# Kernel tuning notes

Hardware: AMD Instinct MI355X
Metric: run time of the kernel (lower is better)

## Reference

```python
import jax, jax.numpy as jnp
import numpy as np

B = 16384       # batch of Monte-Carlo paths
NSTEPS = 32     # time discretization N
H = 128         # hidden width of sub-networks
L = 1.0         # sphere radius l
T1 = 1.0
T0 = 0.0
DT = float((T1 - T0) / NSTEPS)


def _mlp(n, x, W1, b1, W2, b2):
    # sub-network on concat([N, X]): (B,1)+(B,3) -> (B,out)
    inp = jnp.concatenate([n, x], axis=-1)
    h = jnp.tanh(inp @ W1.T + b1)
    return h @ W2.T + b2


def _forward(process_N, process_X, discrete_t, delta_B,
             rW1, rb1, rW2, rb2, gW1, gb1, gW2, gb2, jW1, jb1, jW2, jb2):
    eye = jnp.eye(3, dtype=process_X.dtype)
    alpha = 0.3 * jax.nn.sigmoid(0.1 * process_N)    # birth intensity, (N+1,B,1)
    beta = 0.2 * jax.nn.sigmoid(-0.1 * process_N)    # death intensity, (N+1,B,1)
    u0 = _mlp(process_N[0], process_X[0], rW1, rb1, rW2, rb2)  # result net, (B,1)

    def step(u, xs):
        (Ni, Xi, Np1, ti, dB, ai, bi,
         gW1i, gb1i, gW2i, gb2i, jW1i, jb1i, jW2i, jb2i) = xs
        grad_u = _mlp(Ni, Xi, gW1i, gb1i, gW2i, gb2i)           # (B,3)
        outer = Xi[:, :, None] * Xi[:, None, :] / (L * L)       # (B,3,3)
        sigma = jnp.swapaxes(eye - outer, -2, -1)               # sigma0(X)^T
        T_inv = eye + outer
        k = jnp.sqrt(2.0 / (1.0 + 0.1 * Ni * Ni)) / L           # sqrt(2 D(N))/l, (B,1)
        kg = k * grad_u
        grad_bmm = jnp.einsum('bi,bij,bjk,bk->b', kg, T_inv, sigma, dB)[:, None]
        ui = _mlp(Ni, Xi, jW1i, jb1i, jW2i, jb2i)
        uip = _mlp(Ni + 1.0, Xi, jW1i, jb1i, jW2i, jb2i)
        uim = _mlp(Ni - 1.0, Xi, jW1i, jb1i, jW2i, jb2i)
        dp = uip - ui
        dm = uim - ui
        f = -0.05 * u + 0.05 * jnp.sum(grad_u * Xi, -1, keepdims=True) / L + 0.01 * ti
        u = u + grad_bmm - (ai * dp + bi * dm) * DT - f * DT
        dN = jnp.round(Np1 - Ni)
        u = u + jnp.where(dN > 0, dp, 0.0) + jnp.where(dN < 0, dm, 0.0)
        return u, None

    xs = (process_N[:-1], process_X[:-1], process_N[1:], discrete_t[:-1], delta_B,
          alpha[:-1], beta[:-1], gW1, gb1, gW2, gb2, jW1, jb1, jW2, jb2)
    u, _ = jax.lax.scan(step, u0, xs)
    g = 0.1 * process_N[-1] + jnp.cos(process_X[-1][:, :1])    # terminal condition
    return u, g


def setup_inputs():
    key = jax.random.key(0)
    ks = jax.random.split(key, 16)
    # integer-valued jump process N_t (kept float32), increments in {-1,0,1}
    n0 = jax.random.randint(ks[0], (1, B, 1), 5, 15).astype(jnp.float32)
    jumps = jax.random.randint(ks[1], (NSTEPS, B, 1), -1, 2).astype(jnp.float32)
    process_N = jnp.concatenate([n0, n0 + jnp.cumsum(jumps, axis=0)], axis=0)
    # spatial process on the sphere of radius L
    xr = jax.random.normal(ks[2], (NSTEPS + 1, B, 3), dtype=jnp.float32)
    process_X = L * xr / jnp.linalg.norm(xr, axis=-1, keepdims=True)
    discrete_t = jnp.linspace(T0, T1, NSTEPS + 1, dtype=jnp.float32)
    delta_B = jax.random.normal(ks[3], (NSTEPS, B, 3), dtype=jnp.float32) * float(np.sqrt(DT))

    def lin(k, shape, fan_in):
        return jax.random.normal(k, shape, dtype=jnp.float32) / float(np.sqrt(fan_in))

    rW1 = lin(ks[4], (H, 4), 4);           rb1 = jnp.zeros((H,), jnp.float32)
    rW2 = lin(ks[5], (1, H), H);           rb2 = jnp.zeros((1,), jnp.float32)
    gW1 = lin(ks[6], (NSTEPS, H, 4), 4);   gb1 = jnp.zeros((NSTEPS, H), jnp.float32)
    gW2 = lin(ks[7], (NSTEPS, 3, H), H);   gb2 = jnp.zeros((NSTEPS, 3), jnp.float32)
    jW1 = lin(ks[8], (NSTEPS, H, 4), 4);   jb1 = jnp.zeros((NSTEPS, H), jnp.float32)
    jW2 = lin(ks[9], (NSTEPS, 1, H), H);   jb2 = jnp.zeros((NSTEPS, 1), jnp.float32)
    return dict(process_N=process_N, process_X=process_X, discrete_t=discrete_t,
                delta_B=delta_B, rW1=rW1, rb1=rb1, rW2=rW2, rb2=rb2,
                gW1=gW1, gb1=gb1, gW2=gW2, gb2=gb2,
                jW1=jW1, jb1=jb1, jW2=jW2, jb2=jb2)


def reference(process_N, process_X, discrete_t, delta_B,
              rW1, rb1, rW2, rb2, gW1, gb1, gW2, gb2, jW1, jb1, jW2, jb2):
    return _forward(process_N, process_X, discrete_t, delta_B,
                    rW1, rb1, rW2, rb2, gW1, gb1, gW2, gb2, jW1, jb1, jW2, jb2)
```

## Files before the change

### kernel.cpp

```cpp
#include <hip/hip_runtime.h>
#include <math.h>

#define BB 16384
#define NSTEPS 32
#define HH 128
#define DTF (1.0f/32.0f)
#define SCALE 2.88539008177792681f
#define LOG2E 1.44269504088896340f

typedef float v2f __attribute__((ext_vector_type(2)));
typedef float v16f __attribute__((ext_vector_type(16)));
typedef unsigned int v2u __attribute__((ext_vector_type(2)));

#define SL(v,k) (__builtin_shufflevector((v),(v),2*(k),2*(k)+1))

__device__ __forceinline__ v2f pk_fma(v2f a, v2f b, v2f c) {
    return __builtin_elementwise_fma(a, b, c);
}

__device__ __forceinline__ v2f pk_rcp1(v2f x) {
    v2u xb; __builtin_memcpy(&xb, &x, 8);
    v2u yb = (v2u){0x7EF311C3u, 0x7EF311C3u} - xb;
    v2f y;  __builtin_memcpy(&y, &yb, 8);
    v2f u = pk_fma(-x, y, (v2f){2.0f, 2.0f});
    return y * u;
}

__device__ __forceinline__ float fexp2(float x) {
#if __has_builtin(__builtin_amdgcn_exp2f)
    return __builtin_amdgcn_exp2f(x);
#else
    float r; asm("v_exp_f32 %0, %1" : "=v"(r) : "v"(x)); return r;
#endif
}
__device__ __forceinline__ float frcp(float x) {
#if __has_builtin(__builtin_amdgcn_rcpf)
    return __builtin_amdgcn_rcpf(x);
#else
    float r; asm("v_rcp_f32 %0, %1" : "=v"(r) : "v"(x)); return r;
#endif
}
__device__ __forceinline__ float frsq(float x) {
#if __has_builtin(__builtin_amdgcn_rsqf)
    return __builtin_amdgcn_rsqf(x);
#else
    float r; asm("v_rsq_f32 %0, %1" : "=v"(r) : "v"(x)); return r;
#endif
}

__global__ __launch_bounds__(HH) void xform_kernel(
    const float* __restrict__ gW1, const float* __restrict__ gb1,
    const float* __restrict__ gW2, const float* __restrict__ gb2,
    const float* __restrict__ jW1, const float* __restrict__ jb1,
    const float* __restrict__ jW2,
    float* __restrict__ recA, float* __restrict__ G)
{
    const int i = blockIdx.x;
    const int j = threadIdx.x;
    const int pair = j >> 1;
    const int ln   = j & 1;
    float* r = recA + ((size_t)i*64 + pair)*32;

    const float* gw = gW1 + (size_t)(i*HH + j)*4;
    const float* jw = jW1 + (size_t)(i*HH + j)*4;
    float jw0 = jw[0];
    float g20 = gW2[i*3*HH + 0*HH + j];
    float g21 = gW2[i*3*HH + 1*HH + j];
    float g22 = gW2[i*3*HH + 2*HH + j];

    r[ 0+ln] = SCALE*gw[0];
    r[ 2+ln] = SCALE*gw[1];
    r[ 4+ln] = SCALE*gw[2];
    r[ 6+ln] = SCALE*gw[3];
    r[ 8+ln] = SCALE*gb1[i*HH + j];
    r[10+ln] = -2.0f*g20;
    r[12+ln] = -2.0f*g21;
    r[14+ln] = -2.0f*g22;

    r[16+ln] = SCALE*jw0;
    r[18+ln] = SCALE*jw[1];
    r[20+ln] = SCALE*jw[2];
    r[22+ln] = SCALE*jw[3];
    r[24+ln] = SCALE*jb1[i*HH + j];
    r[26+ln] = -2.0f*jW2[i*HH + j];
    r[28+ln] = exp2f( SCALE*jw0);
    r[30+ln] = exp2f(-SCALE*jw0);

    __shared__ float sh[3*HH];
    sh[0*HH + j] = g20; sh[1*HH + j] = g21; sh[2*HH + j] = g22;
    __syncthreads();
    if (j < 3) {
        float s = gb2[i*3 + j];
        for (int t = 0; t < HH; ++t) s += sh[j*HH + t];
        G[i*4 + j] = s;
    }
}

__global__ __launch_bounds__(256) void step_kernel(
    const float* __restrict__ N, const float* __restrict__ X,
    const float* __restrict__ T, const float* __restrict__ dB,
    const float* __restrict__ recA, const float* __restrict__ G,
    float* __restrict__ C)
{
    const int tid  = threadIdx.x;
    const int i    = blockIdx.x >> 8;
    const int bblk = blockIdx.x & 255;
    const int bl   = tid & 63;
    const int jq   = __builtin_amdgcn_readfirstlane(tid >> 6);
    const int b    = bblk*64 + bl;
    const int ib   = i*BB + b;

    const float Ni = N[ib];
    const float x0 = X[(size_t)ib*3 + 0], x1 = X[(size_t)ib*3 + 1], x2 = X[(size_t)ib*3 + 2];

    const v16f* rec16 = (const v16f*)(recA + (size_t)i*HH*16 + (size_t)jq*512);

    const v2f Niv  = {Ni, Ni};
    const v2f x0v  = {x0, x0};
    const v2f x1v  = {x1, x1};
    const v2f x2v  = {x2, x2};
    const v2f onev = {1.0f, 1.0f};
    const v2f c25v = {25.0f, 25.0f};

    v2f ga0 = {0.f,0.f}, ga1 = {0.f,0.f}, ga2 = {0.f,0.f};
    v2f a0  = {0.f,0.f}, aP  = {0.f,0.f}, aM  = {0.f,0.f};

#pragma unroll 2
    for (int t = 0; t < 16; ++t) {
        const v16f Rg = rec16[2*t + 0];
        const v16f Rj = rec16[2*t + 1];

        v2f ag = SL(Rg,4) * onev;
        ag = pk_fma(SL(Rg,0), Niv, ag);
        ag = pk_fma(SL(Rg,1), x0v, ag);
        ag = pk_fma(SL(Rg,2), x1v, ag);
        ag = pk_fma(SL(Rg,3), x2v, ag);
        ag = __builtin_elementwise_min(ag, c25v);
        v2f eg; eg.x = fexp2(ag.x); eg.y = fexp2(ag.y);
        v2f rg = pk_rcp1(eg + 1.0f);
        ga0 = pk_fma(SL(Rg,5), rg, ga0);
        ga1 = pk_fma(SL(Rg,6), rg, ga1);
        ga2 = pk_fma(SL(Rg,7), rg, ga2);

        v2f aj = SL(Rj,4) * onev;
        aj = pk_fma(SL(Rj,0), Niv, aj);
        aj = pk_fma(SL(Rj,1), x0v, aj);
        aj = pk_fma(SL(Rj,2), x1v, aj);
        aj = pk_fma(SL(Rj,3), x2v, aj);
        aj = __builtin_elementwise_min(aj, c25v);
        v2f ej; ej.x = fexp2(aj.x); ej.y = fexp2(aj.y);
        v2f r0 = pk_rcp1(ej + 1.0f);
        v2f rp = pk_rcp1(pk_fma(SL(Rj,6), ej, onev));
        v2f rm = pk_rcp1(pk_fma(SL(Rj,7), ej, onev));
        const v2f w2p = SL(Rj,5);
        a0 = pk_fma(w2p, r0, a0);
        aP = pk_fma(w2p, rp, aP);
        aM = pk_fma(w2p, rm, aM);
    }

    const float hga0 = ga0.x + ga0.y;
    const float hga1 = ga1.x + ga1.y;
    const float hga2 = ga2.x + ga2.y;
    const float ha0  = a0.x  + a0.y;
    const float haP  = aP.x  + aP.y;
    const float haM  = aM.x  + aM.y;

    __shared__ float sh[3][6][64];
    if (jq) {
        float* s = &sh[jq-1][0][bl];
        s[0*64] = hga0; s[1*64] = hga1; s[2*64] = hga2;
        s[3*64] = ha0;  s[4*64] = haP;  s[5*64] = haM;
    }
    __syncthreads();
    if (!jq) {
        float v0 = hga0, v1 = hga1, v2 = hga2;
        float v3 = ha0,  v4 = haP,  v5 = haM;
#pragma unroll
        for (int q = 0; q < 3; ++q) {
            v0 += sh[q][0][bl]; v1 += sh[q][1][bl]; v2 += sh[q][2][bl];
            v3 += sh[q][3][bl]; v4 += sh[q][4][bl]; v5 += sh[q][5][bl];
        }
        const float g0 = G[i*4 + 0] + v0;
        const float g1 = G[i*4 + 1] + v1;
        const float g2 = G[i*4 + 2] + v2;
        const float A0 = v3;
        const float AP = v4;
        const float AM = v5;

        const float Np1 = N[ib + BB];
        const float d0 = dB[(size_t)ib*3 + 0], d1 = dB[(size_t)ib*3 + 1], d2 = dB[(size_t)ib*3 + 2];
        const float ti = T[i];

        const float gdx = g0*x0 + g1*x1 + g2*x2;
        const float ss  = x0*x0 + x1*x1 + x2*x2;
        const float gdB = g0*d0 + g1*d1 + g2*d2;
        const float xdB = x0*d0 + x1*d1 + x2*d2;

        const float k = 1.41421356237309505f * frsq(fmaf(0.1f*Ni, Ni, 1.0f));
        const float grad_bmm = k * (gdB - ss*gdx*xdB);

        const float dp = AP - A0;
        const float dm = AM - A0;

        const float sig = frcp(1.0f + fexp2(-0.1f*LOG2E*Ni));
        const float alpha = 0.3f*sig;
        const float beta  = 0.2f - 0.2f*sig;

        const float dd = Np1 - Ni;
        const float jump = (dd > 0.5f) ? dp : ((dd < -0.5f) ? dm : 0.0f);

        const float c = grad_bmm - (alpha*dp + beta*dm)*DTF
                      - 0.05f*DTF*gdx - 0.01f*DTF*ti + jump;
        C[ib] = c;
    }
}

__global__ __launch_bounds__(256) void final_kernel(
    const float* __restrict__ N, const float* __restrict__ X,
    const float* __restrict__ rW1, const float* __restrict__ rb1,
    const float* __restrict__ rW2, const float* __restrict__ rb2,
    const float* __restrict__ C, float* __restrict__ out)
{
    const int gid = blockIdx.x*256 + threadIdx.x;
    const int b = gid >> 4;
    const int p = gid & 15;

    const float n0 = N[b];
    const float x0 = X[(size_t)b*3 + 0], x1 = X[(size_t)b*3 + 1], x2 = X[(size_t)b*3 + 2];

    float accw = 0.f, accr = 0.f;
#pragma unroll
    for (int t = 0; t < 8; ++t) {
        const int j = p*8 + t;
        float pre = fmaf(rW1[j*4+0], n0, fmaf(rW1[j*4+1], x0,
                    fmaf(rW1[j*4+2], x1, fmaf(rW1[j*4+3], x2, rb1[j]))));
        float r  = frcp(1.0f + fexp2(SCALE*pre));
        float w2 = rW2[j];
        accw += w2;
        accr = fmaf(w2, r, accr);
    }
    accw += __shfl_down(accw, 8, 16);  accr += __shfl_down(accr, 8, 16);
    accw += __shfl_down(accw, 4, 16);  accr += __shfl_down(accr, 4, 16);
    accw += __shfl_down(accw, 2, 16);  accr += __shfl_down(accr, 2, 16);
    accw += __shfl_down(accw, 1, 16);  accr += __shfl_down(accr, 1, 16);

    if (p == 0) {
        float u = rb2[0] + accw - 2.0f*accr;

        const float sfac = 1.0f + 0.05f*DTF;
#pragma unroll
        for (int i = 0; i < NSTEPS; ++i)
            u = fmaf(u, sfac, C[(size_t)i*BB + b]);
        out[b] = u;

        const int ib = NSTEPS*BB + b;
        out[BB + b] = fmaf(0.1f, N[ib], __cosf(X[(size_t)ib*3]));
    }
}

extern "C" void kernel_launch(void* const* d_in, const int* in_sizes, int n_in,
                              void* d_out, int out_size, void* d_ws, size_t ws_size,
                              hipStream_t stream)
{
    const float* N   = (const float*)d_in[0];
    const float* X   = (const float*)d_in[1];
    const float* T   = (const float*)d_in[2];
    const float* dB  = (const float*)d_in[3];
    const float* rW1 = (const float*)d_in[4];
    const float* rb1 = (const float*)d_in[5];
    const float* rW2 = (const float*)d_in[6];
    const float* rb2 = (const float*)d_in[7];
    const float* gW1 = (const float*)d_in[8];
    const float* gb1 = (const float*)d_in[9];
    const float* gW2 = (const float*)d_in[10];
    const float* gb2 = (const float*)d_in[11];
    const float* jW1 = (const float*)d_in[12];
    const float* jb1 = (const float*)d_in[13];
    const float* jW2 = (const float*)d_in[14];

    float* ws   = (float*)d_ws;
    float* C    = ws;
    float* recA = ws + (size_t)NSTEPS*BB;
    float* G    = recA + (size_t)NSTEPS*HH*16;
    float* out  = (float*)d_out;

    xform_kernel<<<NSTEPS, HH, 0, stream>>>(gW1, gb1, gW2, gb2, jW1, jb1, jW2, recA, G);
    step_kernel<<<NSTEPS*(BB/64), 256, 0, stream>>>(N, X, T, dB, recA, G, C);
    final_kernel<<<BB*16/256, 256, 0, stream>>>(N, X, rW1, rb1, rW2, rb2, C, out);
}
```

Baseline: 63.75 us.

## Split hidden units across 8 waves and parallelize final recurrence and bias reductions

The step kernel now uses 512 threads per block, so each of 8 waves handles 16 hidden units (fully unrolled) instead of 4 waves handling 32, and the shared-memory partial reduction grows to 7 slots. The final kernel replaces the serial 32-step linear recurrence with a closed-form weighted sum: each of 16 lanes loads two C values scaled by precomputed powers of (1+0.05*DT), and the results are reduced with shuffles. The xform kernel's serial bias sum becomes a tree reduction. This buys more latency hiding and shorter per-thread chains at the cost of more block-level reduction work and slightly different floating-point summation order.

```diff
diff --git a/kernel.cpp b/kernel.cpp
--- a/kernel.cpp
+++ b/kernel.cpp
@@ -8,7 +8,7 @@
 #define SCALE 2.88539008177792681f
 #define LOG2E 1.44269504088896340f
 
-typedef float v2f __attribute__((ext_vector_type(2)));
+typedef float v2f  __attribute__((ext_vector_type(2)));
 typedef float v16f __attribute__((ext_vector_type(16)));
 typedef unsigned int v2u __attribute__((ext_vector_type(2)));
 
@@ -87,16 +87,20 @@
     r[30+ln] = exp2f(-SCALE*jw0);
 
     __shared__ float sh[3*HH];
-    sh[0*HH + j] = g20; sh[1*HH + j] = g21; sh[2*HH + j] = g22;
+    sh[j] = g20; sh[HH + j] = g21; sh[2*HH + j] = g22;
     __syncthreads();
-    if (j < 3) {
-        float s = gb2[i*3 + j];
-        for (int t = 0; t < HH; ++t) s += sh[j*HH + t];
-        G[i*4 + j] = s;
-    }
-}
-
-__global__ __launch_bounds__(256) void step_kernel(
+    for (int off = 64; off >= 1; off >>= 1) {
+        if (j < off) {
+            sh[j]      += sh[j + off];
+            sh[HH + j] += sh[HH + j + off];
+            sh[2*HH+j] += sh[2*HH + j + off];
+        }
+        __syncthreads();
+    }
+    if (j < 3) G[i*4 + j] = gb2[i*3 + j] + sh[j*HH];
+}
+
+__global__ __launch_bounds__(512) void step_kernel(
     const float* __restrict__ N, const float* __restrict__ X,
     const float* __restrict__ T, const float* __restrict__ dB,
     const float* __restrict__ recA, const float* __restrict__ G,
@@ -106,14 +110,14 @@
     const int i    = blockIdx.x >> 8;
     const int bblk = blockIdx.x & 255;
     const int bl   = tid & 63;
-    const int jq   = __builtin_amdgcn_readfirstlane(tid >> 6);
+    const int je   = __builtin_amdgcn_readfirstlane(tid >> 6);
     const int b    = bblk*64 + bl;
     const int ib   = i*BB + b;
 
     const float Ni = N[ib];
     const float x0 = X[(size_t)ib*3 + 0], x1 = X[(size_t)ib*3 + 1], x2 = X[(size_t)ib*3 + 2];
 
-    const v16f* rec16 = (const v16f*)(recA + (size_t)i*HH*16 + (size_t)jq*512);
+    const v16f* rec16 = (const v16f*)(recA + (size_t)i*HH*16 + (size_t)je*256);
 
     const v2f Niv  = {Ni, Ni};
     const v2f x0v  = {x0, x0};
@@ -125,31 +129,31 @@
     v2f ga0 = {0.f,0.f}, ga1 = {0.f,0.f}, ga2 = {0.f,0.f};
     v2f a0  = {0.f,0.f}, aP  = {0.f,0.f}, aM  = {0.f,0.f};
 
-#pragma unroll 2
-    for (int t = 0; t < 16; ++t) {
+#pragma unroll
+    for (int t = 0; t < 8; ++t) {
         const v16f Rg = rec16[2*t + 0];
         const v16f Rj = rec16[2*t + 1];
 
-        v2f ag = SL(Rg,4) * onev;
+        v2f ag = SL(Rg,4);
         ag = pk_fma(SL(Rg,0), Niv, ag);
         ag = pk_fma(SL(Rg,1), x0v, ag);
         ag = pk_fma(SL(Rg,2), x1v, ag);
         ag = pk_fma(SL(Rg,3), x2v, ag);
         ag = __builtin_elementwise_min(ag, c25v);
         v2f eg; eg.x = fexp2(ag.x); eg.y = fexp2(ag.y);
-        v2f rg = pk_rcp1(eg + 1.0f);
+        v2f rg = pk_rcp1(eg + onev);
         ga0 = pk_fma(SL(Rg,5), rg, ga0);
         ga1 = pk_fma(SL(Rg,6), rg, ga1);
         ga2 = pk_fma(SL(Rg,7), rg, ga2);
 
-        v2f aj = SL(Rj,4) * onev;
+        v2f aj = SL(Rj,4);
         aj = pk_fma(SL(Rj,0), Niv, aj);
         aj = pk_fma(SL(Rj,1), x0v, aj);
         aj = pk_fma(SL(Rj,2), x1v, aj);
         aj = pk_fma(SL(Rj,3), x2v, aj);
         aj = __builtin_elementwise_min(aj, c25v);
         v2f ej; ej.x = fexp2(aj.x); ej.y = fexp2(aj.y);
-        v2f r0 = pk_rcp1(ej + 1.0f);
+        v2f r0 = pk_rcp1(ej + onev);
         v2f rp = pk_rcp1(pk_fma(SL(Rj,6), ej, onev));
         v2f rm = pk_rcp1(pk_fma(SL(Rj,7), ej, onev));
         const v2f w2p = SL(Rj,5);
@@ -165,27 +169,24 @@
     const float haP  = aP.x  + aP.y;
     const float haM  = aM.x  + aM.y;
 
-    __shared__ float sh[3][6][64];
-    if (jq) {
-        float* s = &sh[jq-1][0][bl];
+    __shared__ float sh[7][6][64];
+    if (je) {
+        float* s = &sh[je-1][0][bl];
         s[0*64] = hga0; s[1*64] = hga1; s[2*64] = hga2;
         s[3*64] = ha0;  s[4*64] = haP;  s[5*64] = haM;
     }
     __syncthreads();
-    if (!jq) {
+    if (!je) {
         float v0 = hga0, v1 = hga1, v2 = hga2;
         float v3 = ha0,  v4 = haP,  v5 = haM;
 #pragma unroll
-        for (int q = 0; q < 3; ++q) {
+        for (int q = 0; q < 7; ++q) {
             v0 += sh[q][0][bl]; v1 += sh[q][1][bl]; v2 += sh[q][2][bl];
             v3 += sh[q][3][bl]; v4 += sh[q][4][bl]; v5 += sh[q][5][bl];
         }
         const float g0 = G[i*4 + 0] + v0;
         const float g1 = G[i*4 + 1] + v1;
         const float g2 = G[i*4 + 2] + v2;
-        const float A0 = v3;
-        const float AP = v4;
-        const float AM = v5;
 
         const float Np1 = N[ib + BB];
         const float d0 = dB[(size_t)ib*3 + 0], d1 = dB[(size_t)ib*3 + 1], d2 = dB[(size_t)ib*3 + 2];
@@ -199,8 +200,8 @@
         const float k = 1.41421356237309505f * frsq(fmaf(0.1f*Ni, Ni, 1.0f));
         const float grad_bmm = k * (gdB - ss*gdx*xdB);
 
-        const float dp = AP - A0;
-        const float dm = AM - A0;
+        const float dp = v4 - v3;
+        const float dm = v5 - v3;
 
         const float sig = frcp(1.0f + fexp2(-0.1f*LOG2E*Ni));
         const float alpha = 0.3f*sig;
@@ -239,22 +240,24 @@
         accw += w2;
         accr = fmaf(w2, r, accr);
     }
-    accw += __shfl_down(accw, 8, 16);  accr += __shfl_down(accr, 8, 16);
-    accw += __shfl_down(accw, 4, 16);  accr += __shfl_down(accr, 4, 16);
-    accw += __shfl_down(accw, 2, 16);  accr += __shfl_down(accr, 2, 16);
-    accw += __shfl_down(accw, 1, 16);  accr += __shfl_down(accr, 1, 16);
+
+    const float l2s = 0.0022524617f;
+    const float wa = fexp2(l2s * (float)(31 - p));
+    const float wb = fexp2(l2s * (float)(15 - p));
+    float csum = fmaf(C[(size_t)p*BB + b], wa, C[(size_t)(p+16)*BB + b] * wb);
+
+    accw += __shfl_down(accw, 8, 16);  accr += __shfl_down(accr, 8, 16);  csum += __shfl_down(csum, 8, 16);
+    accw += __shfl_down(accw, 4, 16);  accr += __shfl_down(accr, 4, 16);  csum += __shfl_down(csum, 4, 16);
+    accw += __shfl_down(accw, 2, 16);  accr += __shfl_down(accr, 2, 16);  csum += __shfl_down(csum, 2, 16);
+    accw += __shfl_down(accw, 1, 16);  accr += __shfl_down(accr, 1, 16);  csum += __shfl_down(csum, 1, 16);
 
     if (p == 0) {
-        float u = rb2[0] + accw - 2.0f*accr;
-
-        const float sfac = 1.0f + 0.05f*DTF;
-#pragma unroll
-        for (int i = 0; i < NSTEPS; ++i)
-            u = fmaf(u, sfac, C[(size_t)i*BB + b]);
-        out[b] = u;
-
-        const int ib = NSTEPS*BB + b;
-        out[BB + b] = fmaf(0.1f, N[ib], __cosf(X[(size_t)ib*3]));
+        float u0 = rb2[0] + accw - 2.0f*accr;
+        const float s32 = 1.05123007f;
+        out[b] = fmaf(u0, s32, csum);
+
+        const int ibl = NSTEPS*BB + b;
+        out[BB + b] = fmaf(0.1f, N[ibl], __cosf(X[(size_t)ibl*3]));
     }
 }
 
@@ -285,6 +288,6 @@
     float* out  = (float*)d_out;
 
     xform_kernel<<<NSTEPS, HH, 0, stream>>>(gW1, gb1, gW2, gb2, jW1, jb1, jW2, recA, G);
-    step_kernel<<<NSTEPS*(BB/64), 256, 0, stream>>>(N, X, T, dB, recA, G, C);
+    step_kernel<<<NSTEPS*(BB/64), 512, 0, stream>>>(N, X, T, dB, recA, G, C);
     final_kernel<<<BB*16/256, 256, 0, stream>>>(N, X, rW1, rb1, rW2, rb2, C, out);
 }
```

Result: slower. 71.56 us (+12.2%).
